# Kernel optimization log

Hardware: AMD Instinct MI355X
Metric: run time of the kernel (lower is better)

Reference implementation:

```python
import jax, jax.numpy as jnp
import numpy as np

N_NODES = 50000


def _gcn_conv(x, row, col, W, b, n_nodes):
    """PyG GCNConv: symmetric-normalized scatter-add aggregation.
    row/col already include self-loops. x: [N, Fin], W: [Fin, Fout]."""
    h = x @ W  # [N, Fout]
    deg = jax.ops.segment_sum(jnp.ones(col.shape[0], x.dtype), col,
                              num_segments=n_nodes)  # in-degree incl. self-loops
    dis = jnp.where(deg > 0, jax.lax.rsqrt(deg), 0.0)  # deg^{-1/2}
    norm = dis[row] * dis[col]  # [E+N]
    msg = h[row] * norm[:, None]  # gather + scale, [E+N, Fout]
    out = jax.ops.segment_sum(msg, col, num_segments=n_nodes)  # scatter-add
    return out + b


def setup_inputs() -> dict:
    key = jax.random.key(0)
    k1, k2, k3, k4 = jax.random.split(key, 4)
    N, E, FIN, FH = N_NODES, 800000, 512, 512
    x = jax.random.normal(k1, (N, FIN), dtype=jnp.float32)
    edge_index = jax.random.randint(k2, (2, E), 0, N, dtype=jnp.int64)
    W1 = jax.random.normal(k3, (FIN, FH), dtype=jnp.float32) * (1.0 / np.sqrt(FIN))
    b1 = jnp.zeros((FH,), jnp.float32)
    W2 = jax.random.normal(k4, (FH, FH), dtype=jnp.float32) * (1.0 / np.sqrt(FH))
    b2 = jnp.zeros((FH,), jnp.float32)
    return {"x": x, "edge_index": edge_index, "W1": W1, "b1": b1,
            "W2": W2, "b2": b2}


def reference(x, edge_index, W1, b1, W2, b2):
    n = x.shape[0]
    loops = jnp.arange(n, dtype=edge_index.dtype)
    row = jnp.concatenate([edge_index[0], loops])  # sources
    col = jnp.concatenate([edge_index[1], loops])  # targets
    h = _gcn_conv(x, row, col, W1, b1, n)
    h = jax.nn.relu(h)
    return _gcn_conv(h, row, col, W2, b2, n)
```

## Files before the change

kernel.cpp:

```cpp
#include <hip/hip_runtime.h>
#include <hip/hip_bf16.h>

typedef short short8 __attribute__((ext_vector_type(8)));
typedef unsigned short u16x8 __attribute__((ext_vector_type(8)));
typedef float f32x4 __attribute__((ext_vector_type(4)));

#define AS1 __attribute__((address_space(1)))
#define AS3 __attribute__((address_space(3)))

__device__ __forceinline__ void gload16(const void* g, void* l) {
  __builtin_amdgcn_global_load_lds((AS1 void*)g, (AS3 void*)l, 16, 0, 0);
}

__device__ __forceinline__ unsigned short f2bf(float f) {
  unsigned u = __float_as_uint(f);
  u = (u + 0x7FFF + ((u >> 16) & 1)) >> 16;
  return (unsigned short)u;
}
__device__ __forceinline__ float bf2f(unsigned short u) {
  return __uint_as_float(((unsigned)u) << 16);
}

__global__ void prep_kernel(const float4* __restrict__ x4, ushort4* __restrict__ xb4, int n4,
                            const float* __restrict__ W1, unsigned short* __restrict__ W1t,
                            const float* __restrict__ W2, unsigned short* __restrict__ W2t) {
  const int nthr = gridDim.x * 256;
  for (int i = blockIdx.x * 256 + threadIdx.x; i < n4; i += nthr) {
    float4 v = x4[i];
    ushort4 o;
    o.x = f2bf(v.x); o.y = f2bf(v.y); o.z = f2bf(v.z); o.w = f2bf(v.w);
    xb4[i] = o;
  }
  for (int idx = blockIdx.x * 256 + threadIdx.x; idx < 512 * 512; idx += nthr) {
    const int k = idx >> 9, n = idx & 511;
    W1t[n * 512 + k] = f2bf(W1[idx]);
    W2t[n * 512 + k] = f2bf(W2[idx]);
  }
}

__global__ void detect64_kernel(const int* __restrict__ ei32, int* __restrict__ flag) {
  const int lane = threadIdx.x;
  const int v = ei32[2 * lane + 1];
  const unsigned long long m = __ballot(v != 0);
  if (lane == 0) *flag = (m == 0ull) ? 1 : 0;
}

__global__ void count_kernel(const int* __restrict__ ei32, const int* __restrict__ flag,
                             int* __restrict__ cnt4, int E, int qdiv) {
  int e = blockIdx.x * 256 + threadIdx.x;
  if (e >= E) return;
  const int is64 = *flag;
  const int r = is64 ? ei32[2 * e] : ei32[e];
  const int c = is64 ? ei32[2 * E + 2 * e] : ei32[E + e];
  int q = r / qdiv; q = q > 3 ? 3 : q;
  atomicAdd(&cnt4[c * 4 + q], 1);
}

__global__ void __launch_bounds__(1024) scan_bsum_kernel(const int* __restrict__ cnt,
                                                         int* __restrict__ bsum, int n) {
  __shared__ int ws[16];
  const int tid = threadIdx.x, lane = tid & 63, wid = tid >> 6;
  const int i = blockIdx.x * 1024 + tid;
  int x = (i < n) ? cnt[i] : 0;
#pragma unroll
  for (int d = 1; d < 64; d <<= 1) x += __shfl_xor(x, d, 64);
  if (lane == 0) ws[wid] = x;
  __syncthreads();
  if (tid == 0) {
    int s = 0;
#pragma unroll
    for (int w = 0; w < 16; ++w) s += ws[w];
    bsum[blockIdx.x] = s;
  }
}

__global__ void __launch_bounds__(1024) scan_boff_kernel(int* __restrict__ bsum,
                                                         int* __restrict__ total, int B) {
  __shared__ int ws[16];
  const int tid = threadIdx.x, lane = tid & 63, wid = tid >> 6;
  const int v = (tid < B) ? bsum[tid] : 0;
  int x = v;
#pragma unroll
  for (int d = 1; d < 64; d <<= 1) {
    int y = __shfl_up(x, d, 64);
    if (lane >= d) x += y;
  }
  if (lane == 63) ws[wid] = x;
  __syncthreads();
  if (tid < 16) {
    int wv = ws[tid];
    int wx = wv;
#pragma unroll
    for (int d = 1; d < 16; d <<= 1) {
      int y = __shfl_up(wx, d, 64);
      if (tid >= d) wx += y;
    }
    ws[tid] = wx - wv;
  }
  __syncthreads();
  const int excl = ws[wid] + (x - v);
  if (tid < B) bsum[tid] = excl;
  if (tid == B - 1) *total = excl + v;
}

__global__ void __launch_bounds__(1024) scan_fill_kernel(const int* __restrict__ cnt,
    const int* __restrict__ boff, int* __restrict__ ptr, int* __restrict__ cur,
    float* __restrict__ dis, int n) {
  __shared__ int ws[16];
  const int tid = threadIdx.x, lane = tid & 63, wid = tid >> 6;
  const int j = blockIdx.x * 1024 + tid;
  const int v = (j < n) ? cnt[j] : 0;
  int x = v;
#pragma unroll
  for (int d = 1; d < 64; d <<= 1) {
    int y = __shfl_up(x, d, 64);
    if (lane >= d) x += y;
  }
  if (lane == 63) ws[wid] = x;
  __syncthreads();
  if (tid < 16) {
    int wv = ws[tid];
    int wx = wv;
#pragma unroll
    for (int d = 1; d < 16; d <<= 1) {
      int y = __shfl_up(wx, d, 64);
      if (tid >= d) wx += y;
    }
    ws[tid] = wx - wv;
  }
  __syncthreads();
  const int v1 = __shfl_down(v, 1, 64);
  const int v2 = __shfl_down(v, 2, 64);
  const int v3 = __shfl_down(v, 3, 64);
  if (j < n) {
    const int excl = boff[blockIdx.x] + ws[wid] + (x - v);
    ptr[j] = excl;
    cur[j] = excl;
    if ((j & 3) == 0) dis[j >> 2] = rsqrtf((float)(v + v1 + v2 + v3 + 1));
  }
}

__global__ void fill_kernel(const int* __restrict__ ei32, const int* __restrict__ flag,
                            int* __restrict__ cur4, int* __restrict__ eidx, int E, int qdiv) {
  int e = blockIdx.x * 256 + threadIdx.x;
  if (e >= E) return;
  const int is64 = *flag;
  const int r = is64 ? ei32[2 * e] : ei32[e];
  const int c = is64 ? ei32[2 * E + 2 * e] : ei32[E + e];
  int q = r / qdiv; q = q > 3 ? 3 : q;
  const int pos = atomicAdd(&cur4[c * 4 + q], 1);
  eidx[pos] = r;
}

template <bool BA, bool BC>
__global__ void __launch_bounds__(256, 3) gemm_kernel(const unsigned short* __restrict__ A,
                                                      const unsigned short* __restrict__ Bt,
                                                      const float* __restrict__ dscale,
                                                      unsigned short* __restrict__ C, int M) {
  __shared__ alignas(128) unsigned short As[8192];
  __shared__ alignas(128) unsigned short Bs[8192];
  const int tid = threadIdx.x;
  const int wave = tid >> 6, lane = tid & 63;
  const int wm = wave >> 1, wn = wave & 1;

  const int nbm = (M + 127) >> 7;
  const int nwg = nbm * 4;
  const int orig = blockIdx.x;
  const int xcd = orig & 7;
  const int q8 = nwg >> 3, r8 = nwg & 7;
  const int wg = (xcd < r8 ? xcd * (q8 + 1) : r8 * (q8 + 1) + (xcd - r8) * q8) + (orig >> 3);
  const int bn = wg & 3;
  const int bm = wg >> 2;

  const int lr = lane >> 3, ls = lane & 7;
  const int fr = lane & 15, ks = lane >> 4;

  f32x4 acc[4][4] = {};

#define STAGE(KO)                                                                          \
  {                                                                                        \
    _Pragma("unroll") for (int i = 0; i < 4; ++i) {                                        \
      int ra = bm * 128 + i * 32 + wave * 8 + lr;                                          \
      ra = ra < M ? ra : M - 1;                                                            \
      const size_t aoff = BA ? ((size_t)(KO)*M + (size_t)ra * 64 + ((ls ^ (lr & 7)) << 3)) \
                             : ((size_t)ra * 512 + (KO) + ((ls ^ (lr & 7)) << 3));         \
      gload16(A + aoff, &As[(i * 32 + wave * 8) * 64]);                                    \
      const int rb = bn * 128 + i * 32 + wave * 8 + lr;                                    \
      gload16(Bt + (size_t)rb * 512 + (KO) + ((ls ^ (lr & 7)) << 3),                       \
              &Bs[(i * 32 + wave * 8) * 64]);                                              \
    }                                                                                      \
  }

  for (int kt = 0; kt < 8; ++kt) {
    if (kt) __syncthreads();
    STAGE(kt * 64)
    __syncthreads();

#pragma unroll
    for (int kk = 0; kk < 2; ++kk) {
      short8 af[4], bfg[4];
#pragma unroll
      for (int m = 0; m < 4; ++m) {
        const int tr = wm * 64 + m * 16 + fr;
        af[m] = *(const short8*)&As[tr * 64 + ((ks * 8 + kk * 32) ^ ((tr & 7) << 3))];
      }
#pragma unroll
      for (int n = 0; n < 4; ++n) {
        const int tb = wn * 64 + n * 16 + fr;
        bfg[n] = *(const short8*)&Bs[tb * 64 + ((ks * 8 + kk * 32) ^ ((tb & 7) << 3))];
      }
#pragma unroll
      for (int m = 0; m < 4; ++m)
#pragma unroll
        for (int n = 0; n < 4; ++n)
          acc[m][n] = __builtin_amdgcn_mfma_f32_16x16x32_bf16(af[m], bfg[n], acc[m][n], 0, 0, 0);
    }
  }
#undef STAGE

  const int rbase = bm * 128 + wm * 64 + (lane >> 4) * 4;
  const int cbase = bn * 128 + wn * 64 + (lane & 15);
  const size_t hseg = (size_t)M * 64;
#pragma unroll
  for (int m = 0; m < 4; ++m)
#pragma unroll
    for (int j = 0; j < 4; ++j) {
      const int r = rbase + m * 16 + j;
      if (r < M) {
        const float ds = dscale[r];
#pragma unroll
        for (int n = 0; n < 4; ++n) {
          const unsigned short val = f2bf(acc[m][n][j] * ds);
          if (BC) {
            const int col = cbase + n * 16;
            C[(size_t)(col >> 6) * hseg + (size_t)r * 64 + (col & 63)] = val;
          } else {
            C[(size_t)r * 512 + cbase + n * 16] = val;
          }
        }
      }
    }
}

template <bool FINAL>
__global__ void __launch_bounds__(256) agg_kernel(const unsigned short* __restrict__ h,
    const int* __restrict__ eidx, const int* __restrict__ ptr4, const float* __restrict__ dis,
    const float* __restrict__ bias, void* __restrict__ outv, int n) {
  const int tid = threadIdx.x;
  const int lane = tid & 63;
  const int slice = blockIdx.x & 7;
  const int g = lane >> 3;
  const int c = lane & 7;
  const int node = (int)(blockIdx.x >> 3) * 32 + (tid >> 6) * 8 + g;
  if (node >= n) return;

  const unsigned short* hs = h + (size_t)slice * ((size_t)n * 64);
  const int coff = c * 8;

  const int start = ptr4[node * 4], end = ptr4[node * 4 + 4];
  float acc[8] = {0, 0, 0, 0, 0, 0, 0, 0};

#define GATH(S) (*(const u16x8*)(hs + (size_t)(unsigned)(S) * 64 + coff))
#define FMA1(V)                                        \
  _Pragma("unroll") for (int j = 0; j < 8; ++j) acc[j] += bf2f((V)[j]);

  int e = start;
  const int alim = min(end, (start + 3) & ~3);
  for (; e < alim; ++e) {
    const u16x8 v = GATH(eidx[e]);
    FMA1(v)
  }
  int4 si;
  if (e + 4 <= end) si = *(const int4*)&eidx[e];
  for (; e + 8 <= end; e += 4) {
    const u16x8 v0 = GATH(si.x), v1 = GATH(si.y), v2 = GATH(si.z), v3 = GATH(si.w);
    si = *(const int4*)&eidx[e + 4];
#pragma unroll
    for (int j = 0; j < 8; ++j)
      acc[j] += bf2f(v0[j]) + bf2f(v1[j]) + bf2f(v2[j]) + bf2f(v3[j]);
  }
  if (e + 4 <= end) {
    const u16x8 v0 = GATH(si.x), v1 = GATH(si.y), v2 = GATH(si.z), v3 = GATH(si.w);
#pragma unroll
    for (int j = 0; j < 8; ++j)
      acc[j] += bf2f(v0[j]) + bf2f(v1[j]) + bf2f(v2[j]) + bf2f(v3[j]);
    e += 4;
  }
  for (; e < end; ++e) {
    const u16x8 v = GATH(eidx[e]);
    FMA1(v)
  }
  {
    const u16x8 v = GATH(node);
    FMA1(v)
  }
#undef FMA1
#undef GATH

  const float di = dis[node];
  const int fcol = slice * 64 + coff;
  float b[8];
  *(float4*)&b[0] = *(const float4*)(bias + fcol);
  *(float4*)&b[4] = *(const float4*)(bias + fcol + 4);

  if (FINAL) {
    float* out = (float*)outv;
    float4 o0, o1;
    o0.x = acc[0] * di + b[0]; o0.y = acc[1] * di + b[1];
    o0.z = acc[2] * di + b[2]; o0.w = acc[3] * di + b[3];
    o1.x = acc[4] * di + b[4]; o1.y = acc[5] * di + b[5];
    o1.z = acc[6] * di + b[6]; o1.w = acc[7] * di + b[7];
    *(float4*)(out + (size_t)node * 512 + fcol) = o0;
    *(float4*)(out + (size_t)node * 512 + fcol + 4) = o1;
  } else {
    unsigned short* out = (unsigned short*)outv;
    u16x8 o;
#pragma unroll
    for (int j = 0; j < 8; ++j) {
      const float t = acc[j] * di + b[j];
      o[j] = f2bf(t > 0.0f ? t : 0.0f);
    }
    *(u16x8*)(out + (size_t)slice * ((size_t)n * 64) + (size_t)node * 64 + coff) = o;
  }
}

extern "C" void kernel_launch(void* const* d_in, const int* in_sizes, int n_in,
                              void* d_out, int out_size, void* d_ws, size_t ws_size,
                              hipStream_t stream) {
  const float* x  = (const float*)d_in[0];
  const int*   ei = (const int*)d_in[1];
  const float* W1 = (const float*)d_in[2];
  const float* b1 = (const float*)d_in[3];
  const float* W2 = (const float*)d_in[4];
  const float* b2 = (const float*)d_in[5];
  float* out = (float*)d_out;

  const int M = in_sizes[0] / 512;
  const int E = in_sizes[1] / 2;
  const int qdiv = (M + 3) >> 2;

  auto alignup = [](size_t v) { return (v + 255) & ~(size_t)255; };
  char* p = (char*)d_ws;
  unsigned short* xb  = (unsigned short*)p; p += alignup((size_t)M * 512 * 2);
  unsigned short* h1b = (unsigned short*)p; p += alignup((size_t)M * 512 * 2);
  unsigned short* r1b = (unsigned short*)p; p += alignup((size_t)M * 512 * 2);
  unsigned short* w1b = (unsigned short*)p; p += alignup(512 * 512 * 2);
  unsigned short* w2b = (unsigned short*)p; p += alignup(512 * 512 * 2);
  float* dis = (float*)p; p += alignup((size_t)M * 4);
  int* ptr4  = (int*)p;   p += alignup(((size_t)M * 4 + 1) * 4);
  int* eidx  = (int*)p;   p += alignup((size_t)E * 4);
  int* flag  = (int*)p;   p += alignup(256);
  int* bsum  = (int*)p;   p += alignup(1024);
  int* cnt4 = (int*)h1b;
  int* cur4 = (int*)((char*)h1b + alignup((size_t)M * 16));
  unsigned short* h2b = xb;

  const int n4 = M * 4;
  hipMemsetAsync(cnt4, 0, (size_t)n4 * 4, stream);
  detect64_kernel<<<1, 64, 0, stream>>>(ei, flag);

  prep_kernel<<<2048, 256, 0, stream>>>((const float4*)x, (ushort4*)xb, M * 128,
                                        W1, w1b, W2, w2b);

  const int B = (n4 + 1023) / 1024;
  count_kernel<<<(E + 255) / 256, 256, 0, stream>>>(ei, flag, cnt4, E, qdiv);
  scan_bsum_kernel<<<B, 1024, 0, stream>>>(cnt4, bsum, n4);
  scan_boff_kernel<<<1, 1024, 0, stream>>>(bsum, ptr4 + n4, B);
  scan_fill_kernel<<<B, 1024, 0, stream>>>(cnt4, bsum, ptr4, cur4, dis, n4);
  fill_kernel<<<(E + 255) / 256, 256, 0, stream>>>(ei, flag, cur4, eidx, E, qdiv);

  const int nwg = ((M + 127) / 128) * 4;
  const int nag = ((M + 31) / 32) * 8;
  gemm_kernel<false, true><<<nwg, 256, 0, stream>>>(xb, w1b, dis, h1b, M);
  agg_kernel<false><<<nag, 256, 0, stream>>>(h1b, eidx, ptr4, dis, b1, (void*)r1b, M);
  gemm_kernel<true, true><<<nwg, 256, 0, stream>>>(r1b, w2b, dis, h2b, M);
  agg_kernel<true><<<nag, 256, 0, stream>>>(h2b, eidx, ptr4, dis, b2, (void*)out, M);
}
```

Baseline: 368.5 us.

## Double-buffer GEMM LDS tiles and store CSR edge indices as 16-bit

The GEMM now keeps two LDS buffers per operand, so the async global-to-LDS loads for the next K tile are issued before computing on the current one. This overlaps memory traffic with MFMA work instead of stalling between stages. LDS use doubles, and the launch bound drops to two blocks per CU. Separately, the CSR source-index array is narrowed from int32 to uint16, halving index traffic in the fill and aggregation kernels. This is only correct while the node count stays below 65536.

New measurement: 370.4 us. About the same (+0.5%).

```diff
diff --git a/kernel.cpp b/kernel.cpp
--- a/kernel.cpp
+++ b/kernel.cpp
@@ -141,7 +141,8 @@
 }
 
 __global__ void fill_kernel(const int* __restrict__ ei32, const int* __restrict__ flag,
-                            int* __restrict__ cur4, int* __restrict__ eidx, int E, int qdiv) {
+                            int* __restrict__ cur4, unsigned short* __restrict__ eidx16,
+                            int E, int qdiv) {
   int e = blockIdx.x * 256 + threadIdx.x;
   if (e >= E) return;
   const int is64 = *flag;
@@ -149,16 +150,16 @@
   const int c = is64 ? ei32[2 * E + 2 * e] : ei32[E + e];
   int q = r / qdiv; q = q > 3 ? 3 : q;
   const int pos = atomicAdd(&cur4[c * 4 + q], 1);
-  eidx[pos] = r;
+  eidx16[pos] = (unsigned short)r;
 }
 
 template <bool BA, bool BC>
-__global__ void __launch_bounds__(256, 3) gemm_kernel(const unsigned short* __restrict__ A,
+__global__ void __launch_bounds__(256, 2) gemm_kernel(const unsigned short* __restrict__ A,
                                                       const unsigned short* __restrict__ Bt,
                                                       const float* __restrict__ dscale,
                                                       unsigned short* __restrict__ C, int M) {
-  __shared__ alignas(128) unsigned short As[8192];
-  __shared__ alignas(128) unsigned short Bs[8192];
+  __shared__ alignas(128) unsigned short As[2][8192];
+  __shared__ alignas(128) unsigned short Bs[2][8192];
   const int tid = threadIdx.x;
   const int wave = tid >> 6, lane = tid & 63;
   const int wm = wave >> 1, wn = wave & 1;
@@ -177,24 +178,32 @@
 
   f32x4 acc[4][4] = {};
 
-#define STAGE(KO)                                                                          \
+#define STAGE(BUF, KO)                                                                     \
   {                                                                                        \
     _Pragma("unroll") for (int i = 0; i < 4; ++i) {                                        \
       int ra = bm * 128 + i * 32 + wave * 8 + lr;                                          \
       ra = ra < M ? ra : M - 1;                                                            \
       const size_t aoff = BA ? ((size_t)(KO)*M + (size_t)ra * 64 + ((ls ^ (lr & 7)) << 3)) \
                              : ((size_t)ra * 512 + (KO) + ((ls ^ (lr & 7)) << 3));         \
-      gload16(A + aoff, &As[(i * 32 + wave * 8) * 64]);                                    \
+      gload16(A + aoff, &As[BUF][(i * 32 + wave * 8) * 64]);                               \
       const int rb = bn * 128 + i * 32 + wave * 8 + lr;                                    \
       gload16(Bt + (size_t)rb * 512 + (KO) + ((ls ^ (lr & 7)) << 3),                       \
-              &Bs[(i * 32 + wave * 8) * 64]);                                              \
+              &Bs[BUF][(i * 32 + wave * 8) * 64]);                                         \
     }                                                                                      \
   }
 
+  STAGE(0, 0)
+
+  int buf = 0;
   for (int kt = 0; kt < 8; ++kt) {
-    if (kt) __syncthreads();
-    STAGE(kt * 64)
-    __syncthreads();
+    if (kt < 7) {
+      STAGE(buf ^ 1, (kt + 1) * 64)
+      asm volatile("s_waitcnt vmcnt(8)" ::: "memory");
+    } else {
+      asm volatile("s_waitcnt vmcnt(0)" ::: "memory");
+    }
+    __builtin_amdgcn_s_barrier();
+    asm volatile("" ::: "memory");
 
 #pragma unroll
     for (int kk = 0; kk < 2; ++kk) {
@@ -202,12 +211,12 @@
 #pragma unroll
       for (int m = 0; m < 4; ++m) {
         const int tr = wm * 64 + m * 16 + fr;
-        af[m] = *(const short8*)&As[tr * 64 + ((ks * 8 + kk * 32) ^ ((tr & 7) << 3))];
+        af[m] = *(const short8*)&As[buf][tr * 64 + ((ks * 8 + kk * 32) ^ ((tr & 7) << 3))];
       }
 #pragma unroll
       for (int n = 0; n < 4; ++n) {
         const int tb = wn * 64 + n * 16 + fr;
-        bfg[n] = *(const short8*)&Bs[tb * 64 + ((ks * 8 + kk * 32) ^ ((tb & 7) << 3))];
+        bfg[n] = *(const short8*)&Bs[buf][tb * 64 + ((ks * 8 + kk * 32) ^ ((tb & 7) << 3))];
       }
 #pragma unroll
       for (int m = 0; m < 4; ++m)
@@ -215,6 +224,10 @@
         for (int n = 0; n < 4; ++n)
           acc[m][n] = __builtin_amdgcn_mfma_f32_16x16x32_bf16(af[m], bfg[n], acc[m][n], 0, 0, 0);
     }
+
+    asm volatile("" ::: "memory");
+    __builtin_amdgcn_s_barrier();
+    buf ^= 1;
   }
 #undef STAGE
 
@@ -244,8 +257,9 @@
 
 template <bool FINAL>
 __global__ void __launch_bounds__(256) agg_kernel(const unsigned short* __restrict__ h,
-    const int* __restrict__ eidx, const int* __restrict__ ptr4, const float* __restrict__ dis,
-    const float* __restrict__ bias, void* __restrict__ outv, int n) {
+    const unsigned short* __restrict__ eidx16, const int* __restrict__ ptr4,
+    const float* __restrict__ dis, const float* __restrict__ bias, void* __restrict__ outv,
+    int n) {
   const int tid = threadIdx.x;
   const int lane = tid & 63;
   const int slice = blockIdx.x & 7;
@@ -267,14 +281,14 @@
   int e = start;
   const int alim = min(end, (start + 3) & ~3);
   for (; e < alim; ++e) {
-    const u16x8 v = GATH(eidx[e]);
+    const u16x8 v = GATH(eidx16[e]);
     FMA1(v)
   }
-  int4 si;
-  if (e + 4 <= end) si = *(const int4*)&eidx[e];
+  ushort4 si;
+  if (e + 4 <= end) si = *(const ushort4*)&eidx16[e];
   for (; e + 8 <= end; e += 4) {
     const u16x8 v0 = GATH(si.x), v1 = GATH(si.y), v2 = GATH(si.z), v3 = GATH(si.w);
-    si = *(const int4*)&eidx[e + 4];
+    si = *(const ushort4*)&eidx16[e + 4];
 #pragma unroll
     for (int j = 0; j < 8; ++j)
       acc[j] += bf2f(v0[j]) + bf2f(v1[j]) + bf2f(v2[j]) + bf2f(v3[j]);
@@ -287,7 +301,7 @@
     e += 4;
   }
   for (; e < end; ++e) {
-    const u16x8 v = GATH(eidx[e]);
+    const u16x8 v = GATH(eidx16[e]);
     FMA1(v)
   }
   {
@@ -348,7 +362,7 @@
   unsigned short* w2b = (unsigned short*)p; p += alignup(512 * 512 * 2);
   float* dis = (float*)p; p += alignup((size_t)M * 4);
   int* ptr4  = (int*)p;   p += alignup(((size_t)M * 4 + 1) * 4);
-  int* eidx  = (int*)p;   p += alignup((size_t)E * 4);
+  unsigned short* eidx16 = (unsigned short*)p; p += alignup((size_t)E * 2);
   int* flag  = (int*)p;   p += alignup(256);
   int* bsum  = (int*)p;   p += alignup(1024);
   int* cnt4 = (int*)h1b;
@@ -367,12 +381,12 @@
   scan_bsum_kernel<<<B, 1024, 0, stream>>>(cnt4, bsum, n4);
   scan_boff_kernel<<<1, 1024, 0, stream>>>(bsum, ptr4 + n4, B);
   scan_fill_kernel<<<B, 1024, 0, stream>>>(cnt4, bsum, ptr4, cur4, dis, n4);
-  fill_kernel<<<(E + 255) / 256, 256, 0, stream>>>(ei, flag, cur4, eidx, E, qdiv);
+  fill_kernel<<<(E + 255) / 256, 256, 0, stream>>>(ei, flag, cur4, eidx16, E, qdiv);
 
   const int nwg = ((M + 127) / 128) * 4;
   const int nag = ((M + 31) / 32) * 8;
   gemm_kernel<false, true><<<nwg, 256, 0, stream>>>(xb, w1b, dis, h1b, M);
-  agg_kernel<false><<<nag, 256, 0, stream>>>(h1b, eidx, ptr4, dis, b1, (void*)r1b, M);
+  agg_kernel<false><<<nag, 256, 0, stream>>>(h1b, eidx16, ptr4, dis, b1, (void*)r1b, M);
   gemm_kernel<true, true><<<nwg, 256, 0, stream>>>(r1b, w2b, dis, h2b, M);
-  agg_kernel<true><<<nag, 256, 0, stream>>>(h2b, eidx, ptr4, dis, b2, (void*)out, M);
-}
+  agg_kernel<true><<<nag, 256, 0, stream>>>(h2b, eidx16, ptr4, dis, b2, (void*)out, M);
+}
```
